# Performance work log

Hardware: AMD Instinct MI355X
Metric: run time of the kernel (lower is better)

Reference implementation:

```python
import jax, jax.numpy as jnp
import numpy as np

N_NODES, N_EDGES, HID = 30000, 480000, 128
N_GRAPHS, N_CLASSES = 128, 6
BN_EPS, ADD_SCORE = 1e-5, 0.5


def setup_inputs():
    key = jax.random.key(0)
    ks = jax.random.split(key, 12)
    g = lambda i, shape: jax.random.normal(ks[i], shape, jnp.float32) * 0.05
    return dict(
        x=jax.random.normal(ks[0], (N_NODES, HID), jnp.float32),
        edge_index=jax.random.randint(ks[1], (2, N_EDGES), 0, N_NODES, jnp.int32),
        batch=jnp.sort(jax.random.randint(ks[2], (N_NODES,), 0, N_GRAPHS, jnp.int32)),
        Wl=g(3, (6, HID, HID)), bl=jnp.zeros((6, HID), jnp.float32),
        Wr=g(4, (6, HID, HID)),
        gamma=jnp.ones((6, HID), jnp.float32), beta=jnp.zeros((6, HID), jnp.float32),
        Wlin=g(5, (3, HID, 2 * HID)), blin=jnp.zeros((3, HID), jnp.float32),
        Wp=g(6, (3, 2 * HID)), bp=jnp.zeros((3,), jnp.float32),
        Wf1=g(7, (HID, HID)), bf1=jnp.zeros((HID,), jnp.float32),
        Wf2=g(8, (N_CLASSES, HID)), bf2=jnp.zeros((N_CLASSES,), jnp.float32),
    )


def _sage(x, src, dst, emf, Wl_i, bl_i, Wr_i, N):
    # PyG SAGEConv: lin_l(mean_{j->i} x_j) + lin_r(x_i); emf masks dead edges
    msg = x[src] * emf[:, None]                              # [E,H]
    s = jax.ops.segment_sum(msg, dst, num_segments=N)
    c = jax.ops.segment_sum(emf, dst, num_segments=N)
    mean = s / jnp.maximum(c, 1.0)[:, None]
    return mean @ Wl_i.T + bl_i + x @ Wr_i.T


def _bn(x, g, b, nvf):
    # training-mode BatchNorm over valid (non-merged-away) nodes only
    cnt = jnp.maximum(nvf.sum(), 1.0)
    mu = (x * nvf[:, None]).sum(0) / cnt
    var = (((x - mu) ** 2) * nvf[:, None]).sum(0) / cnt
    return g * (x - mu) * jax.lax.rsqrt(var + BN_EPS) + b


def _edge_pool(x, src, dst, emb, nvb, Wp_i, bp_i, N, E):
    h = x.shape[1]
    # raw edge score = Linear(cat(x[src], x[dst]))
    raw = (x @ Wp_i[:h])[src] + (x @ Wp_i[h:])[dst] + bp_i   # [E]
    neg = jnp.finfo(x.dtype).min
    mx = jax.ops.segment_max(jnp.where(emb, raw, neg), dst, num_segments=N)
    z = jnp.where(emb, jnp.exp(jnp.where(emb, raw - mx[dst], 0.0)), 0.0)
    den = jax.ops.segment_sum(z, dst, num_segments=N)
    score = z / jnp.maximum(den, 1e-16)[dst] + ADD_SCORE     # softmax per dst + 0.5

    # greedy edge matching in descending score order (sequential, int-only carry)
    order = jnp.argsort(-jnp.where(emb, jax.lax.stop_gradient(score), -jnp.inf))

    def step(carry, i):
        matched, cluster, chosen = carry
        s, t = src[i], dst[i]
        ok = emb[i] & (~matched[s]) & (~matched[t]) & (s != t)
        rep, oth = jnp.minimum(s, t), jnp.maximum(s, t)
        matched = matched.at[s].set(matched[s] | ok)
        matched = matched.at[t].set(matched[t] | ok)
        cluster = cluster.at[oth].set(jnp.where(ok, rep, cluster[oth]))
        chosen = chosen.at[rep].set(jnp.where(ok, i, chosen[rep]))
        return (matched, cluster, chosen), None

    init = (~nvb, jnp.arange(N, dtype=jnp.int32), jnp.full((N,), -1, jnp.int32))
    (matched, cluster, chosen), _ = jax.lax.scan(step, init, order)

    # merged node = (x_s + x_t) * score(chosen edge); singleton score = 1
    nscore = jnp.where(chosen >= 0, score[jnp.maximum(chosen, 0)], 1.0)
    new_x = jax.ops.segment_sum(x, cluster, num_segments=N) * nscore[:, None]
    nvb2 = nvb & (cluster == jnp.arange(N, dtype=jnp.int32))
    # remap edges to cluster representatives; coalesce duplicates (self-loops kept, as PyG)
    key = jnp.where(emb, cluster[src] * N + cluster[dst], -1)  # N*N < 2**31
    uk = jnp.unique(key, size=E, fill_value=-1)
    emb2 = uk >= 0
    ukc = jnp.maximum(uk, 0)
    return new_x, ukc // N, ukc % N, emb2, nvb2


def reference(x, edge_index, batch, Wl, bl, Wr, gamma, beta, Wlin, blin, Wp, bp, Wf1, bf1, Wf2, bf2):
    N, E = x.shape[0], edge_index.shape[1]
    src, dst = edge_index[0], edge_index[1]
    emb = jnp.ones((E,), bool)   # edge-valid mask (fixed-shape graph coarsening)
    nvb = jnp.ones((N,), bool)   # node-valid mask
    for blk in range(3):
        emf, nvf = emb.astype(x.dtype), nvb.astype(x.dtype)
        i = 2 * blk
        h = _bn(jax.nn.relu(_sage(x, src, dst, emf, Wl[i], bl[i], Wr[i], N)), gamma[i], beta[i], nvf)
        h2 = _bn(jax.nn.relu(_sage(h, src, dst, emf, Wl[i + 1], bl[i + 1], Wr[i + 1], N)), gamma[i + 1], beta[i + 1], nvf)
        x = jnp.concatenate([h2, h], axis=1) @ Wlin[blk].T + blin[blk]  # dropout = identity (eval)
        x, src, dst, emb, nvb = _edge_pool(x, src, dst, emb, nvb, Wp[blk], bp[blk], N, E)
    nvf = nvb.astype(x.dtype)
    sums = jax.ops.segment_sum(x * nvf[:, None], batch, num_segments=N_GRAPHS)
    cnt = jax.ops.segment_sum(nvf, batch, num_segments=N_GRAPHS)
    pooled = sums / jnp.maximum(cnt, 1.0)[:, None]           # global_mean_pool
    hfc = jax.nn.relu(pooled @ Wf1.T + bf1)
    return jax.nn.log_softmax(hfc @ Wf2.T + bf2, axis=1)
```

## Files before the change

kernel.cpp:

```cpp
#include <hip/hip_runtime.h>
#include <stdint.h>

#define NN 30000
#define NE 480000
#define HID 128
#define NG 128
#define NC 6
#define BN_EPS 1e-5f
#define WPB 938
#define SLOTS 4
#define GPAD 132

typedef unsigned int u32;
typedef unsigned long long u64;

__device__ __forceinline__ u64 ent_key(int4 ent) {
  return ((u64)(u32)ent.y << 32) | (u32)ent.x;
}

__global__ void k_init(const int* __restrict__ ei, int* srcA, int* dstA, int* nvb,
                       int* scal, int* b3, int* i2, float* gbuf,
                       double* __restrict__ bnsum) {
  int t = blockIdx.x * 256 + threadIdx.x;
  if (t < NE) { srcA[t] = ei[t]; dstA[t] = ei[NE + t]; }
  if (t < NN) nvb[t] = 1;
  if (t < 2 * NN) { b3[t] = 0; i2[t] = 0; }
  if (t < NG * HID + NG) gbuf[t] = 0.f;
  if (t < 2 * HID) bnsum[t] = 0.0;
  if (t == 0) { scal[0] = NE; scal[1] = 0; }
}

__global__ void k_csr_count(const int* __restrict__ pE, const int* __restrict__ src,
                            const int* __restrict__ dst, int* __restrict__ cnt,
                            int* __restrict__ icnt, const int* __restrict__ nvb,
                            int* __restrict__ pcnt) {
  int t = blockIdx.x * 256 + threadIdx.x;
  if (t < NN && nvb[t]) atomicAdd(pcnt, 1);
  if (t < *pE) {
    int s = src[t], d = dst[t];
    atomicAdd(&cnt[d], 1);
    if (s != d) { atomicAdd(&icnt[s], 1); atomicAdd(&icnt[d], 1); }
  }
}

__global__ __launch_bounds__(1024) void k_scan2(const int* __restrict__ in0, int* __restrict__ out0,
                                                const int* __restrict__ in1, int* __restrict__ out1) {
  const int* in = blockIdx.x ? in1 : in0;
  int* out = blockIdx.x ? out1 : out0;
  __shared__ int part[1024];
  int t = threadIdx.x;
  int chunk = (NN + 1023) / 1024;
  int b = t * chunk, e = b + chunk;
  if (b > NN) b = NN;
  if (e > NN) e = NN;
  int s = 0;
  for (int i = b; i < e; i++) s += in[i];
  part[t] = s;
  __syncthreads();
  for (int off = 1; off < 1024; off <<= 1) {
    int v = (t >= off) ? part[t - off] : 0;
    __syncthreads();
    part[t] += v;
    __syncthreads();
  }
  int excl = (t == 0) ? 0 : part[t - 1];
  for (int i = b; i < e; i++) { out[i] = excl; excl += in[i]; }
  if (t == 0) out[NN] = part[1023];
}

__global__ void k_csr_scatter(const int* __restrict__ pE, const int* __restrict__ src,
                              const int* __restrict__ dst, const int* __restrict__ coff,
                              int* __restrict__ cursor, int* __restrict__ eids,
                              int* __restrict__ gsrc) {
  int e = blockIdx.x * 256 + threadIdx.x;
  if (e >= *pE) return;
  int d = dst[e];
  int pos = coff[d] + atomicAdd(&cursor[d], 1);
  eids[pos] = e;
  gsrc[pos] = src[e];
}

__global__ __launch_bounds__(256) void k_sage_gather(
    const int* __restrict__ coff, const int* __restrict__ gsrc,
    const float* __restrict__ x, float* __restrict__ mean) {
  int grp = threadIdx.x >> 5;
  int lane = threadIdx.x & 31;
  int n = blockIdx.x * 8 + grp;
  if (n >= NN) return;
  int b = coff[n], e2 = coff[n + 1];
  float4 acc = make_float4(0.f, 0.f, 0.f, 0.f);
  int i = b;
  for (; i + 1 < e2; i += 2) {
    int s0 = gsrc[i], s1 = gsrc[i + 1];
    float4 v0 = *(const float4*)(x + (size_t)s0 * HID + lane * 4);
    float4 v1 = *(const float4*)(x + (size_t)s1 * HID + lane * 4);
    acc.x += v0.x; acc.y += v0.y; acc.z += v0.z; acc.w += v0.w;
    acc.x += v1.x; acc.y += v1.y; acc.z += v1.z; acc.w += v1.w;
  }
  if (i < e2) {
    int s0 = gsrc[i];
    float4 v0 = *(const float4*)(x + (size_t)s0 * HID + lane * 4);
    acc.x += v0.x; acc.y += v0.y; acc.z += v0.z; acc.w += v0.w;
  }
  float inv = 1.0f / fmaxf((float)(e2 - b), 1.0f);
  acc.x *= inv; acc.y *= inv; acc.z *= inv; acc.w *= inv;
  *(float4*)(mean + (size_t)n * HID + lane * 4) = acc;
}

__global__ __launch_bounds__(256) void gemm_dual2(
    const float* __restrict__ A1, const float* __restrict__ W1,
    const float* __restrict__ A2, const float* __restrict__ W2,
    const float* __restrict__ bias, float* __restrict__ out,
    int M, int ldw, int relu, const int* __restrict__ nvb,
    double* __restrict__ bnsum, int dostats,
    const float* __restrict__ a1f, const float* __restrict__ c1f,
    const float* __restrict__ a2f, const float* __restrict__ c2f,
    const float* __restrict__ Wp, float* __restrict__ px1, float* __restrict__ px2) {
  __shared__ float Ast[16][GPAD];
  __shared__ float Ws[16][GPAD];
  int tid = threadIdx.x;
  int rg = tid >> 4, cg = tid & 15;
  int r0 = rg * 8, c0 = cg * 8;
  int row0 = blockIdx.x * 128;
  float acc[8][8];
#pragma unroll
  for (int a = 0; a < 8; a++)
#pragma unroll
    for (int bq = 0; bq < 8; bq++) acc[a][bq] = 0.f;

  for (int srcI = 0; srcI < 2; srcI++) {
    const float* A = srcI ? A2 : A1;
    const float* W = srcI ? W2 : W1;
    const float* fa = srcI ? a2f : a1f;
    const float* fc = srcI ? c2f : c1f;
    for (int kc = 0; kc < 128; kc += 16) {
#pragma unroll
      for (int i = 0; i < 2; i++) {
        int k = tid + i * 256;
        int r = k >> 2, c4 = (k & 3) << 2;
        int gr = row0 + r;
        float4 v = make_float4(0.f, 0.f, 0.f, 0.f);
        if (gr < M) v = *(const float4*)(A + (size_t)gr * 128 + kc + c4);
        if (fa) {
          float4 av = *(const float4*)(fa + kc + c4);
          float4 cv = *(const float4*)(fc + kc + c4);
          v.x = v.x * av.x + cv.x; v.y = v.y * av.y + cv.y;
          v.z = v.z * av.z + cv.z; v.w = v.w * av.w + cv.w;
        }
        Ast[c4 + 0][r] = v.x; Ast[c4 + 1][r] = v.y;
        Ast[c4 + 2][r] = v.z; Ast[c4 + 3][r] = v.w;
        float4 w = *(const float4*)(W + (size_t)r * ldw + kc + c4);
        Ws[c4 + 0][r] = w.x; Ws[c4 + 1][r] = w.y;
        Ws[c4 + 2][r] = w.z; Ws[c4 + 3][r] = w.w;
      }
      __syncthreads();
#pragma unroll
      for (int kk = 0; kk < 16; kk++) {
        float4 a0 = *(const float4*)(&Ast[kk][r0]);
        float4 a1 = *(const float4*)(&Ast[kk][r0 + 4]);
        float4 b0 = *(const float4*)(&Ws[kk][c0]);
        float4 b1 = *(const float4*)(&Ws[kk][c0 + 4]);
        float av[8] = {a0.x, a0.y, a0.z, a0.w, a1.x, a1.y, a1.z, a1.w};
        float bv[8] = {b0.x, b0.y, b0.z, b0.w, b1.x, b1.y, b1.z, b1.w};
#pragma unroll
        for (int rr = 0; rr < 8; rr++)
#pragma unroll
          for (int cc = 0; cc < 8; cc++) acc[rr][cc] += av[rr] * bv[cc];
      }
      __syncthreads();
    }
  }

  float wp1[8], wp2[8];
  if (Wp) {
#pragma unroll
    for (int cc = 0; cc < 8; cc++) { wp1[cc] = Wp[c0 + cc]; wp2[cc] = Wp[HID + c0 + cc]; }
  }
  float* part1 = (float*)Ast;
  float* part2 = (float*)Ws;
  float sCol[8], qCol[8];
#pragma unroll
  for (int cc = 0; cc < 8; cc++) { sCol[cc] = 0.f; qCol[cc] = 0.f; }
#pragma unroll
  for (int rr = 0; rr < 8; rr++) {
    int gr = row0 + r0 + rr;
    float p1 = 0.f, p2 = 0.f;
    if (gr < M) {
      int valid = dostats ? nvb[gr] : 0;
      float vv[8];
#pragma unroll
      for (int cc = 0; cc < 8; cc++) {
        float v = acc[rr][cc] + bias[c0 + cc];
        if (relu) v = fmaxf(v, 0.f);
        vv[cc] = v;
        if (valid) { sCol[cc] += v; qCol[cc] += v * v; }
        if (Wp) { p1 += v * wp1[cc]; p2 += v * wp2[cc]; }
      }
      *(float4*)(out + (size_t)gr * 128 + c0) = make_float4(vv[0], vv[1], vv[2], vv[3]);
      *(float4*)(out + (size_t)gr * 128 + c0 + 4) = make_float4(vv[4], vv[5], vv[6], vv[7]);
    }
    if (Wp) { part1[(r0 + rr) * 16 + cg] = p1; part2[(r0 + rr) * 16 + cg] = p2; }
  }
  if (Wp) {
    __syncthreads();
    if (tid < HID && row0 + tid < M) {
      float s1 = 0.f, s2 = 0.f;
#pragma unroll
      for (int g = 0; g < 16; g++) { s1 += part1[tid * 16 + g]; s2 += part2[tid * 16 + g]; }
      px1[row0 + tid] = s1;
      px2[row0 + tid] = s2;
    }
  }
  if (dostats) {
#pragma unroll
    for (int cc = 0; cc < 8; cc++) { Ast[rg][c0 + cc] = sCol[cc]; Ws[rg][c0 + cc] = qCol[cc]; }
    __syncthreads();
    if (tid < HID) {
      float s = 0.f, q = 0.f;
#pragma unroll
      for (int g = 0; g < 16; g++) { s += Ast[g][tid]; q += Ws[g][tid]; }
      atomicAdd(&bnsum[tid], (double)s);
      atomicAdd(&bnsum[HID + tid], (double)q);
    }
  }
}

__global__ void k_bnfold(double* __restrict__ bnsum, const int* __restrict__ cnt,
                         const float* __restrict__ gamma, const float* __restrict__ beta,
                         float* __restrict__ affa, float* __restrict__ affc) {
  int k = threadIdx.x;
  double c = (double)((*cnt > 1) ? *cnt : 1);
  double mu = bnsum[k] / c;
  double var = bnsum[HID + k] / c - mu * mu;
  if (var < 0.0) var = 0.0;
  double inv = 1.0 / sqrt(var + (double)BN_EPS);
  double a = (double)gamma[k] * inv;
  affa[k] = (float)a;
  affc[k] = (float)((double)beta[k] - mu * a);
  bnsum[k] = 0.0;
  bnsum[HID + k] = 0.0;
}

__global__ void k_edge_softmax_seed(
    const int* __restrict__ coff, const int* __restrict__ eids,
    const int* __restrict__ gsrc, const float* __restrict__ px1,
    const float* __restrict__ px2, const float* __restrict__ bp,
    float* __restrict__ score, u64* __restrict__ ekey, u64* __restrict__ S) {
  int n = blockIdx.x * 256 + threadIdx.x;
  if (n >= NN) return;
  S[n] = 0ull;
  int b = coff[n], e2 = coff[n + 1];
  if (b == e2) return;
  float p2 = px2[n] + *bp;
  float mx = -3.4e38f;
  for (int i = b; i < e2; i++) {
    float r = px1[gsrc[i]] + p2;
    mx = fmaxf(mx, r);
  }
  double den = 0.0;
  for (int i = b; i < e2; i++) {
    int eid = eids[i];
    float z = expf(px1[gsrc[i]] + p2 - mx);
    score[eid] = z;
    den += (double)z;
  }
  if (den < 1e-16) den = 1e-16;
  double invd = 1.0 / den;
  for (int i = b; i < e2; i++) {
    int eid = eids[i];
    float sc = (float)((double)score[eid] * invd) + 0.5f;
    score[eid] = sc;
    ekey[eid] = ((u64)__float_as_uint(sc) << 32) | (u64)(0xFFFFFFFFu - (u32)eid);
  }
}

__global__ void k_inc_scatter(const int* __restrict__ pE, const int* __restrict__ src,
                              const int* __restrict__ dst, const u64* __restrict__ ekey,
                              const int* __restrict__ ioff, int* __restrict__ icur,
                              int4* __restrict__ ielist) {
  int e = blockIdx.x * 256 + threadIdx.x;
  if (e >= *pE) return;
  int s = src[e], d = dst[e];
  if (s == d) return;
  u64 k = ekey[e];
  int4 ent;
  ent.x = (int)(u32)(k & 0xFFFFFFFFull);
  ent.y = (int)(u32)(k >> 32);
  ent.w = 0;
  ent.z = d;
  ielist[ioff[s] + atomicAdd(&icur[s], 1)] = ent;
  ent.z = s;
  ielist[ioff[d] + atomicAdd(&icur[d], 1)] = ent;
}

__global__ __launch_bounds__(256) void k_suitor(
    const int* __restrict__ ioff, const int4* __restrict__ ielist,
    const int* __restrict__ src, const int* __restrict__ dst,
    u64* __restrict__ S) {
  int wid = threadIdx.x >> 6;
  int lane = threadIdx.x & 63;
  int n = blockIdx.x * 4 + wid;
  if (n >= NN) return;
  int cur = n;
  while (cur >= 0) {
    int b = ioff[cur], e2 = ioff[cur + 1];
    int deg = e2 - b;
    if (deg == 0) break;
    if (deg <= 64 * SLOTS) {
      u64 key[SLOTS]; int pv[SLOTS];
#pragma unroll
      for (int s = 0; s < SLOTS; s++) {
        key[s] = 0; pv[s] = 0;
        int i = b + s * 64 + lane;
        if (i < e2) {
          int4 ent = ielist[i];
          key[s] = ent_key(ent);
          pv[s] = ent.z;
        }
      }
      long long res;
      for (;;) {
        u64 localBest = 0;
#pragma unroll
        for (int s = 0; s < SLOTS; s++) {
          if (!key[s]) continue;
          u64 sv = __hip_atomic_load(&S[pv[s]], __ATOMIC_RELAXED, __HIP_MEMORY_SCOPE_AGENT);
          if (sv >= key[s]) key[s] = 0;
          else if (key[s] > localBest) localBest = key[s];
        }
        u64 bestKey = localBest;
#pragma unroll
        for (int o = 32; o > 0; o >>= 1) {
          u64 other = __shfl_xor(bestKey, o, 64);
          if (other > bestKey) bestKey = other;
        }
        if (bestKey == 0) { res = -1; break; }
        int ms = -1;
#pragma unroll
        for (int s = 0; s < SLOTS; s++)
          if (ms < 0 && key[s] == bestKey) ms = s;
        u64 ball = __ballot(ms >= 0);
        int owner = (int)(__ffsll((long long)ball) - 1);
        long long r0 = -3;
        if (lane == owner) {
          int bv = pv[ms];
          u64 old = atomicMax(&S[bv], bestKey);
          if (old >= bestKey) { key[ms] = 0; r0 = -2; }
          else if (old == 0) r0 = -1;
          else {
            int eo = (int)(0xFFFFFFFFu - (u32)(old & 0xFFFFFFFFull));
            int so = src[eo], do_ = dst[eo];
            r0 = (so == bv) ? do_ : so;
          }
        }
        res = __shfl(r0, owner, 64);
        if (res != -2) break;
      }
      if (res < 0) break;
      cur = (int)res;
    } else {
      u64 bestKey = 0;
      for (int i = b + lane; i < e2; i += 64) {
        int4 ent = ielist[i];
        u64 k = ent_key(ent);
        if (k <= bestKey) continue;
        u64 sv = __hip_atomic_load(&S[ent.z], __ATOMIC_RELAXED, __HIP_MEMORY_SCOPE_AGENT);
        if (k > sv) bestKey = k;
      }
#pragma unroll
      for (int o = 32; o > 0; o >>= 1) {
        u64 other = __shfl_xor(bestKey, o, 64);
        if (other > bestKey) bestKey = other;
      }
      long long r0 = -1;
      if (bestKey != 0 && lane == 0) {
        int e = (int)(0xFFFFFFFFu - (u32)(bestKey & 0xFFFFFFFFull));
        int es = src[e], ed = dst[e];
        int bv = (es == cur) ? ed : es;
        u64 old = atomicMax(&S[bv], bestKey);
        if (old >= bestKey) r0 = cur;
        else if (old != 0) {
          int eo = (int)(0xFFFFFFFFu - (u32)(old & 0xFFFFFFFFull));
          int so = src[eo], do_ = dst[eo];
          r0 = (so == bv) ? do_ : so;
        }
      }
      long long res = (bestKey != 0) ? __shfl(r0, 0, 64) : -1;
      cur = (int)res;
    }
  }
}

__global__ __launch_bounds__(256) void k_new_x(
    const u64* __restrict__ S, const int* __restrict__ src, const int* __restrict__ dst,
    const float* __restrict__ score, const float* __restrict__ x,
    float* __restrict__ out, int* __restrict__ cluster,
    int* __restrict__ nvb, int* __restrict__ b3zero) {
  int gt = blockIdx.x * 256 + threadIdx.x;
  if (gt < 2 * NN) b3zero[gt] = 0;
  int grp = threadIdx.x >> 5;
  int lane = threadIdx.x & 31;
  int n = blockIdx.x * 8 + grp;
  if (n >= NN) return;
  u64 k = S[n];
  int partner = -1;
  int rep = n;
  bool isOth = false;
  float sc = 1.f;
  if (k) {
    int e = (int)(0xFFFFFFFFu - (u32)(k & 0xFFFFFFFFull));
    int s = src[e], d = dst[e];
    int other = (s == n) ? d : s;
    if (S[other] == k) {
      if (n > other) { isOth = true; rep = other; }
      else { partner = other; sc = score[e]; }
    }
  }
  float4 v = make_float4(0.f, 0.f, 0.f, 0.f);
  if (!isOth) {
    v = *(const float4*)(x + (size_t)n * HID + lane * 4);
    if (partner >= 0) {
      float4 w = *(const float4*)(x + (size_t)partner * HID + lane * 4);
      v.x = (v.x + w.x) * sc; v.y = (v.y + w.y) * sc;
      v.z = (v.z + w.z) * sc; v.w = (v.w + w.w) * sc;
    }
  }
  *(float4*)(out + (size_t)n * HID + lane * 4) = v;
  if (lane == 0) {
    cluster[n] = rep;
    nvb[n] = (nvb[n] && !isOth) ? 1 : 0;
  }
}

__global__ void k_bucket_count(const int* __restrict__ pE, const int* __restrict__ src,
                               const int* __restrict__ cluster, int* __restrict__ bcount) {
  int e = blockIdx.x * 256 + threadIdx.x;
  if (e >= *pE) return;
  atomicAdd(&bcount[cluster[src[e]]], 1);
}

__global__ __launch_bounds__(1024) void k_scan(const int* __restrict__ in, int* __restrict__ out,
                                               int n, int* totalDst) {
  __shared__ int part[1024];
  int t = threadIdx.x;
  int chunk = (n + 1023) / 1024;
  int b = t * chunk, e = b + chunk;
  if (b > n) b = n;
  if (e > n) e = n;
  int s = 0;
  for (int i = b; i < e; i++) s += in[i];
  part[t] = s;
  __syncthreads();
  for (int off = 1; off < 1024; off <<= 1) {
    int v = (t >= off) ? part[t - off] : 0;
    __syncthreads();
    part[t] += v;
    __syncthreads();
  }
  int excl = (t == 0) ? 0 : part[t - 1];
  int total = part[1023];
  for (int i = b; i < e; i++) { out[i] = excl; excl += in[i]; }
  if (t == 0) {
    out[n] = total;
    if (totalDst) *totalDst = total;
  }
}

__global__ void k_bucket_scatter(const int* __restrict__ pE, const int* __restrict__ src,
                                 const int* __restrict__ dst, const int* __restrict__ cluster,
                                 const int* __restrict__ boffs, int* __restrict__ bcursor,
                                 int* __restrict__ bucket) {
  int e = blockIdx.x * 256 + threadIdx.x;
  if (e >= *pE) return;
  int cs = cluster[src[e]], cd = cluster[dst[e]];
  int pos = boffs[cs] + atomicAdd(&bcursor[cs], 1);
  bucket[pos] = cd;
}

__global__ __launch_bounds__(256) void k_dedup_bitmap(
    const int* __restrict__ boffs, int* __restrict__ bucket,
    int* __restrict__ ucount) {
  __shared__ u32 bm[4][960];
  int wid = threadIdx.x >> 6;
  int lane = threadIdx.x & 63;
  int n = blockIdx.x * 4 + wid;
  int b = boffs[n], e = boffs[n + 1];
  for (int w = lane; w < 960; w += 64) bm[wid][w] = 0;
  __syncthreads();
  for (int i = b + lane; i < e; i += 64)
    atomicOr(&bm[wid][bucket[i] >> 5], 1u << (bucket[i] & 31));
  __syncthreads();
  int w0 = lane * 15;
  int w1 = w0 + 15; if (w1 > WPB) w1 = WPB;
  int cnt = 0;
  for (int w = w0; w < w1; w++) cnt += __popc(bm[wid][w]);
  int inc = cnt;
  for (int o = 1; o < 64; o <<= 1) { int v = __shfl_up(inc, o); if (lane >= o) inc += v; }
  int excl = inc - cnt;
  int total = __shfl(inc, 63);
  int pos = b + excl;
  for (int w = w0; w < w1; w++) {
    u32 v = bm[wid][w];
    while (v) { int bit = __ffs(v) - 1; bucket[pos++] = (w << 5) | bit; v &= v - 1; }
  }
  if (lane == 0) ucount[n] = total;
}

__global__ void k_emit(const int* __restrict__ boffs, const int* __restrict__ bucket,
                       const int* __restrict__ bucount, const int* __restrict__ bnoffs,
                       int* __restrict__ srcO, int* __restrict__ dstO,
                       int* __restrict__ b3zero, int* __restrict__ i2zero,
                       int* __restrict__ pcnt) {
  int t = blockIdx.x * 256 + threadIdx.x;
  int stride = gridDim.x * 256;
  for (int z = t; z < 2 * NN; z += stride) { b3zero[z] = 0; i2zero[z] = 0; }
  if (t == 0) *pcnt = 0;
  if (t >= NN) return;
  int u = bucount[t], b = boffs[t], o = bnoffs[t];
  for (int i = 0; i < u; i++) { srcO[o + i] = t; dstO[o + i] = bucket[b + i]; }
}

__global__ void k_graph_pool(const int* __restrict__ nvb, const int* __restrict__ batch,
                             const float* __restrict__ x, float* __restrict__ gsum,
                             float* __restrict__ gcnt) {
  int t = blockIdx.x * 256 + threadIdx.x;
  int n = t >> 2;
  if (n >= NN) return;
  if (!nvb[n]) return;
  int sub = t & 3;
  int g = batch[n];
  const float* xr = x + (size_t)n * HID + sub * 32;
  float* o = gsum + (size_t)g * HID + sub * 32;
#pragma unroll
  for (int i = 0; i < 8; i++) {
    float4 v = *(const float4*)(xr + i * 4);
    atomicAdd(o + i * 4 + 0, v.x); atomicAdd(o + i * 4 + 1, v.y);
    atomicAdd(o + i * 4 + 2, v.z); atomicAdd(o + i * 4 + 3, v.w);
  }
  if (sub == 0) atomicAdd(&gcnt[g], 1.0f);
}

__global__ __launch_bounds__(128) void k_head1(const float* __restrict__ gsum,
                                               const float* __restrict__ gcnt,
                                               const float* __restrict__ Wf1,
                                               const float* __restrict__ bf1,
                                               float* __restrict__ hfc) {
  int g = blockIdx.x;
  int j = threadIdx.x;
  __shared__ float p[HID];
  float c = fmaxf(gcnt[g], 1.f);
  p[j] = gsum[g * HID + j] / c;
  __syncthreads();
  float s = bf1[j];
  const float* w = Wf1 + (size_t)j * HID;
  for (int k = 0; k < HID; k++) s += p[k] * w[k];
  hfc[g * HID + j] = fmaxf(s, 0.f);
}

__global__ void k_head2(const float* __restrict__ hfc, const float* __restrict__ Wf2,
                        const float* __restrict__ bf2, float* __restrict__ out) {
  int g = blockIdx.x;
  int t = threadIdx.x;
  __shared__ float lg[NC];
  if (t < NC) {
    float s = bf2[t];
    const float* w = Wf2 + (size_t)t * HID;
    const float* h = hfc + (size_t)g * HID;
    for (int k = 0; k < HID; k++) s += h[k] * w[k];
    lg[t] = s;
  }
  __syncthreads();
  if (t == 0) {
    float m = lg[0];
    for (int c = 1; c < NC; c++) m = fmaxf(m, lg[c]);
    float se = 0.f;
    for (int c = 0; c < NC; c++) se += expf(lg[c] - m);
    float lse = m + logf(se);
    for (int c = 0; c < NC; c++) out[g * NC + c] = lg[c] - lse;
  }
}

extern "C" void kernel_launch(void* const* d_in, const int* in_sizes, int n_in,
                              void* d_out, int out_size, void* d_ws, size_t ws_size,
                              hipStream_t stream) {
  const float* x0 = (const float*)d_in[0];
  const int* ei = (const int*)d_in[1];
  const int* batch = (const int*)d_in[2];
  const float* Wl = (const float*)d_in[3];
  const float* bl = (const float*)d_in[4];
  const float* Wr = (const float*)d_in[5];
  const float* gamma = (const float*)d_in[6];
  const float* beta = (const float*)d_in[7];
  const float* Wlin = (const float*)d_in[8];
  const float* blin = (const float*)d_in[9];
  const float* Wp = (const float*)d_in[10];
  const float* bp = (const float*)d_in[11];
  const float* Wf1 = (const float*)d_in[12];
  const float* bf1 = (const float*)d_in[13];
  const float* Wf2 = (const float*)d_in[14];
  const float* bf2 = (const float*)d_in[15];
  float* out = (float*)d_out;

  const int NH = NN * HID;
  size_t off = 0;
  char* base = (char*)d_ws;
  auto carve = [&](size_t bytes) -> char* {
    char* p = base + off;
    off += (bytes + 255) & ~(size_t)255;
    return p;
  };
  float* xa = (float*)carve((size_t)NH * 4);
  float* xb = (float*)carve((size_t)NH * 4);
  float* xc = (float*)carve((size_t)NH * 4);
  float* xd = (float*)carve((size_t)NH * 4);
  int* srcA = (int*)carve((size_t)NE * 4);
  int* dstA = (int*)carve((size_t)NE * 4);
  int* srcB = (int*)carve((size_t)NE * 4);
  int* dstB = (int*)carve((size_t)NE * 4);
  float* escore = (float*)carve((size_t)NE * 4);
  int* ebucket = (int*)carve((size_t)NE * 4);
  int* eids = (int*)carve((size_t)NE * 4);
  int* gsrc = (int*)carve((size_t)NE * 4);
  u64* ekey = (u64*)carve((size_t)NE * 8);
  u64* S = (u64*)carve((size_t)NN * 8);
  float* npx1 = (float*)carve((size_t)NN * 4);
  float* npx2 = (float*)carve((size_t)NN * 4);
  int* ncluster = (int*)carve((size_t)NN * 4);
  int* nvb = (int*)carve((size_t)NN * 4);
  int* b3 = (int*)carve((size_t)3 * NN * 4);
  int* bcount = b3;
  int* bcursor = b3 + NN;
  int* bucount = b3 + 2 * NN;
  int* i2 = (int*)carve((size_t)2 * NN * 4);
  int* icnt = i2;
  int* icursor = i2 + NN;
  int* boffs = (int*)carve((size_t)(NN + 1) * 4);
  int* bnoffs = (int*)carve((size_t)(NN + 1) * 4);
  int* csroff = (int*)carve((size_t)(NN + 1) * 4);
  int* ioff = (int*)carve((size_t)(NN + 1) * 4);
  double* bnsum = (double*)carve((size_t)2 * HID * 8);
  float* affa1 = (float*)carve((size_t)HID * 4);
  float* affc1 = (float*)carve((size_t)HID * 4);
  float* affa2 = (float*)carve((size_t)HID * 4);
  float* affc2 = (float*)carve((size_t)HID * 4);
  float* gbuf = (float*)carve((size_t)(NG * HID + NG) * 4);
  float* gsum = gbuf;
  float* gcnt = gbuf + NG * HID;
  float* ghfc = (float*)carve((size_t)NG * HID * 4);
  int* scal = (int*)carve(64 * 4);
  (void)ws_size; (void)n_in; (void)in_sizes; (void)out_size;

  int4* ielist = (int4*)xc;

  int* pE = scal;
  int* pcnt = scal + 1;

  k_init<<<1875, 256, 0, stream>>>(ei, srcA, dstA, nvb, scal, b3, i2, gbuf, bnsum);

  int* srcC = srcA; int* dstC = dstA; int* srcN = srcB; int* dstN = dstB;
  float* xcur = xa;
  float* xtmp = xd;

  auto sage = [&](const float* xin, float* xout, int L, const float* fa, const float* fc) {
    k_sage_gather<<<3750, 256, 0, stream>>>(csroff, gsrc, xin, xtmp);
    gemm_dual2<<<235, 256, 0, stream>>>(xtmp, Wl + (size_t)L * HID * HID, xin,
                                        Wr + (size_t)L * HID * HID, bl + (size_t)L * HID,
                                        xout, NN, HID, 1, nvb, bnsum, 1,
                                        fa, fc, fa, fc, nullptr, nullptr, nullptr);
  };

  for (int b = 0; b < 3; b++) {
    const float* xin = (b == 0) ? x0 : (const float*)xcur;

    k_csr_count<<<1875, 256, 0, stream>>>(pE, srcC, dstC, bcount, icnt, nvb, pcnt);
    k_scan2<<<2, 1024, 0, stream>>>(bcount, csroff, icnt, ioff);
    k_csr_scatter<<<1875, 256, 0, stream>>>(pE, srcC, dstC, csroff, bcursor, eids, gsrc);

    sage(xin, xb, 2 * b, nullptr, nullptr);
    k_bnfold<<<1, 128, 0, stream>>>(bnsum, pcnt, gamma + (size_t)(2 * b) * HID,
                                    beta + (size_t)(2 * b) * HID, affa1, affc1);
    sage(xb, xc, 2 * b + 1, affa1, affc1);
    k_bnfold<<<1, 128, 0, stream>>>(bnsum, pcnt, gamma + (size_t)(2 * b + 1) * HID,
                                    beta + (size_t)(2 * b + 1) * HID, affa2, affc2);
    gemm_dual2<<<235, 256, 0, stream>>>(xc, Wlin + (size_t)b * HID * 2 * HID, xb,
                                        Wlin + (size_t)b * HID * 2 * HID + HID,
                                        blin + (size_t)b * HID, xcur, NN, 2 * HID, 0,
                                        nvb, bnsum, 0, affa2, affc2, affa1, affc1,
                                        Wp + (size_t)b * 2 * HID, npx1, npx2);

    k_edge_softmax_seed<<<118, 256, 0, stream>>>(csroff, eids, gsrc, npx1, npx2, bp + b,
                                                 escore, ekey, S);
    k_inc_scatter<<<1875, 256, 0, stream>>>(pE, srcC, dstC, ekey, ioff, icursor, ielist);
    k_suitor<<<7500, 256, 0, stream>>>(ioff, ielist, srcC, dstC, S);
    k_new_x<<<3750, 256, 0, stream>>>(S, srcC, dstC, escore, xcur, xtmp,
                                      ncluster, nvb, b3);

    if (b < 2) {
      k_bucket_count<<<1875, 256, 0, stream>>>(pE, srcC, ncluster, bcount);
      k_scan<<<1, 1024, 0, stream>>>(bcount, boffs, NN, (int*)nullptr);
      k_bucket_scatter<<<1875, 256, 0, stream>>>(pE, srcC, dstC, ncluster, boffs, bcursor,
                                                 ebucket);
      k_dedup_bitmap<<<7500, 256, 0, stream>>>(boffs, ebucket, bucount);
      k_scan<<<1, 1024, 0, stream>>>(bucount, bnoffs, NN, pE);
      k_emit<<<235, 256, 0, stream>>>(boffs, ebucket, bucount, bnoffs, srcN, dstN,
                                      b3, i2, pcnt);
      { int* t = srcC; srcC = srcN; srcN = t; t = dstC; dstC = dstN; dstN = t; }
    }
    { float* t = xcur; xcur = xtmp; xtmp = t; }
  }

  k_graph_pool<<<469, 256, 0, stream>>>(nvb, batch, xcur, gsum, gcnt);
  k_head1<<<NG, 128, 0, stream>>>(gsum, gcnt, Wf1, bf1, ghfc);
  k_head2<<<NG, 32, 0, stream>>>(ghfc, Wf2, bf2, out);
}
```

Before: 2.504 ms.

## Fuse incidence scatter into softmax kernel and CSR counting into edge emit

Removes the separate k_inc_scatter pass and the ekey buffer by writing incidence-list entries directly from the per-node softmax loop. Degree counting for the next block's CSR moves into k_emit and runs once up front for block 0, so the per-block k_csr_count launch goes away. The valid-node counter is now maintained in k_new_x (reset in the softmax kernel), and zeroing of b3/i2 moves into the dedup kernel. This saves launches and edge-array passes, but the scatter now runs node-serially in 118 blocks and emit does per-edge atomics in a serial per-node loop, which may reduce parallelism.

```diff
diff --git a/kernel.cpp b/kernel.cpp
--- a/kernel.cpp
+++ b/kernel.cpp
@@ -27,20 +27,17 @@
   if (t < 2 * NN) { b3[t] = 0; i2[t] = 0; }
   if (t < NG * HID + NG) gbuf[t] = 0.f;
   if (t < 2 * HID) bnsum[t] = 0.0;
-  if (t == 0) { scal[0] = NE; scal[1] = 0; }
+  if (t == 0) { scal[0] = NE; scal[1] = NN; }
 }
 
 __global__ void k_csr_count(const int* __restrict__ pE, const int* __restrict__ src,
                             const int* __restrict__ dst, int* __restrict__ cnt,
-                            int* __restrict__ icnt, const int* __restrict__ nvb,
-                            int* __restrict__ pcnt) {
-  int t = blockIdx.x * 256 + threadIdx.x;
-  if (t < NN && nvb[t]) atomicAdd(pcnt, 1);
-  if (t < *pE) {
-    int s = src[t], d = dst[t];
-    atomicAdd(&cnt[d], 1);
-    if (s != d) { atomicAdd(&icnt[s], 1); atomicAdd(&icnt[d], 1); }
-  }
+                            int* __restrict__ icnt) {
+  int e = blockIdx.x * 256 + threadIdx.x;
+  if (e >= *pE) return;
+  int s = src[e], d = dst[e];
+  atomicAdd(&cnt[d], 1);
+  if (s != d) { atomicAdd(&icnt[s], 1); atomicAdd(&icnt[d], 1); }
 }
 
 __global__ __launch_bounds__(1024) void k_scan2(const int* __restrict__ in0, int* __restrict__ out0,
@@ -245,8 +242,11 @@
     const int* __restrict__ coff, const int* __restrict__ eids,
     const int* __restrict__ gsrc, const float* __restrict__ px1,
     const float* __restrict__ px2, const float* __restrict__ bp,
-    float* __restrict__ score, u64* __restrict__ ekey, u64* __restrict__ S) {
+    float* __restrict__ score, u64* __restrict__ S,
+    const int* __restrict__ ioff, int* __restrict__ icur,
+    int4* __restrict__ ielist, int* __restrict__ pcnt) {
   int n = blockIdx.x * 256 + threadIdx.x;
+  if (blockIdx.x == 0 && threadIdx.x == 0) *pcnt = 0;
   if (n >= NN) return;
   S[n] = 0ull;
   int b = coff[n], e2 = coff[n + 1];
@@ -270,27 +270,18 @@
     int eid = eids[i];
     float sc = (float)((double)score[eid] * invd) + 0.5f;
     score[eid] = sc;
-    ekey[eid] = ((u64)__float_as_uint(sc) << 32) | (u64)(0xFFFFFFFFu - (u32)eid);
-  }
-}
-
-__global__ void k_inc_scatter(const int* __restrict__ pE, const int* __restrict__ src,
-                              const int* __restrict__ dst, const u64* __restrict__ ekey,
-                              const int* __restrict__ ioff, int* __restrict__ icur,
-                              int4* __restrict__ ielist) {
-  int e = blockIdx.x * 256 + threadIdx.x;
-  if (e >= *pE) return;
-  int s = src[e], d = dst[e];
-  if (s == d) return;
-  u64 k = ekey[e];
-  int4 ent;
-  ent.x = (int)(u32)(k & 0xFFFFFFFFull);
-  ent.y = (int)(u32)(k >> 32);
-  ent.w = 0;
-  ent.z = d;
-  ielist[ioff[s] + atomicAdd(&icur[s], 1)] = ent;
-  ent.z = s;
-  ielist[ioff[d] + atomicAdd(&icur[d], 1)] = ent;
+    int s = gsrc[i];
+    if (s == n) continue;
+    u64 k = ((u64)__float_as_uint(sc) << 32) | (u64)(0xFFFFFFFFu - (u32)eid);
+    int4 ent;
+    ent.x = (int)(u32)(k & 0xFFFFFFFFull);
+    ent.y = (int)(u32)(k >> 32);
+    ent.w = 0;
+    ent.z = s;
+    ielist[ioff[n] + atomicAdd(&icur[n], 1)] = ent;
+    ent.z = n;
+    ielist[ioff[s] + atomicAdd(&icur[s], 1)] = ent;
+  }
 }
 
 __global__ __launch_bounds__(256) void k_suitor(
@@ -395,7 +386,7 @@
     const u64* __restrict__ S, const int* __restrict__ src, const int* __restrict__ dst,
     const float* __restrict__ score, const float* __restrict__ x,
     float* __restrict__ out, int* __restrict__ cluster,
-    int* __restrict__ nvb, int* __restrict__ b3zero) {
+    int* __restrict__ nvb, int* __restrict__ b3zero, int* __restrict__ pcnt) {
   int gt = blockIdx.x * 256 + threadIdx.x;
   if (gt < 2 * NN) b3zero[gt] = 0;
   int grp = threadIdx.x >> 5;
@@ -428,7 +419,9 @@
   *(float4*)(out + (size_t)n * HID + lane * 4) = v;
   if (lane == 0) {
     cluster[n] = rep;
-    nvb[n] = (nvb[n] && !isOth) ? 1 : 0;
+    int nv = (nvb[n] && !isOth) ? 1 : 0;
+    nvb[n] = nv;
+    if (nv) atomicAdd(pcnt, 1);
   }
 }
 
@@ -479,7 +472,9 @@
 
 __global__ __launch_bounds__(256) void k_dedup_bitmap(
     const int* __restrict__ boffs, int* __restrict__ bucket,
-    int* __restrict__ ucount) {
+    int* __restrict__ ucount, int* __restrict__ b3zero, int* __restrict__ i2zero) {
+  int gt = blockIdx.x * 256 + threadIdx.x;
+  for (int z = gt; z < 2 * NN; z += gridDim.x * 256) { b3zero[z] = 0; i2zero[z] = 0; }
   __shared__ u32 bm[4][960];
   int wid = threadIdx.x >> 6;
   int lane = threadIdx.x & 63;
@@ -509,15 +504,17 @@
 __global__ void k_emit(const int* __restrict__ boffs, const int* __restrict__ bucket,
                        const int* __restrict__ bucount, const int* __restrict__ bnoffs,
                        int* __restrict__ srcO, int* __restrict__ dstO,
-                       int* __restrict__ b3zero, int* __restrict__ i2zero,
-                       int* __restrict__ pcnt) {
+                       int* __restrict__ cnt, int* __restrict__ icnt) {
   int t = blockIdx.x * 256 + threadIdx.x;
-  int stride = gridDim.x * 256;
-  for (int z = t; z < 2 * NN; z += stride) { b3zero[z] = 0; i2zero[z] = 0; }
-  if (t == 0) *pcnt = 0;
   if (t >= NN) return;
   int u = bucount[t], b = boffs[t], o = bnoffs[t];
-  for (int i = 0; i < u; i++) { srcO[o + i] = t; dstO[o + i] = bucket[b + i]; }
+  for (int i = 0; i < u; i++) {
+    int d = bucket[b + i];
+    srcO[o + i] = t;
+    dstO[o + i] = d;
+    atomicAdd(&cnt[d], 1);
+    if (t != d) { atomicAdd(&icnt[t], 1); atomicAdd(&icnt[d], 1); }
+  }
 }
 
 __global__ void k_graph_pool(const int* __restrict__ nvb, const int* __restrict__ batch,
@@ -621,7 +618,6 @@
   int* ebucket = (int*)carve((size_t)NE * 4);
   int* eids = (int*)carve((size_t)NE * 4);
   int* gsrc = (int*)carve((size_t)NE * 4);
-  u64* ekey = (u64*)carve((size_t)NE * 8);
   u64* S = (u64*)carve((size_t)NN * 8);
   float* npx1 = (float*)carve((size_t)NN * 4);
   float* npx2 = (float*)carve((size_t)NN * 4);
@@ -656,6 +652,7 @@
   int* pcnt = scal + 1;
 
   k_init<<<1875, 256, 0, stream>>>(ei, srcA, dstA, nvb, scal, b3, i2, gbuf, bnsum);
+  k_csr_count<<<1875, 256, 0, stream>>>(pE, srcA, dstA, bcount, icnt);
 
   int* srcC = srcA; int* dstC = dstA; int* srcN = srcB; int* dstN = dstB;
   float* xcur = xa;
@@ -672,7 +669,6 @@
   for (int b = 0; b < 3; b++) {
     const float* xin = (b == 0) ? x0 : (const float*)xcur;
 
-    k_csr_count<<<1875, 256, 0, stream>>>(pE, srcC, dstC, bcount, icnt, nvb, pcnt);
     k_scan2<<<2, 1024, 0, stream>>>(bcount, csroff, icnt, ioff);
     k_csr_scatter<<<1875, 256, 0, stream>>>(pE, srcC, dstC, csroff, bcursor, eids, gsrc);
 
@@ -689,21 +685,20 @@
                                         Wp + (size_t)b * 2 * HID, npx1, npx2);
 
     k_edge_softmax_seed<<<118, 256, 0, stream>>>(csroff, eids, gsrc, npx1, npx2, bp + b,
-                                                 escore, ekey, S);
-    k_inc_scatter<<<1875, 256, 0, stream>>>(pE, srcC, dstC, ekey, ioff, icursor, ielist);
+                                                 escore, S, ioff, icursor, ielist, pcnt);
     k_suitor<<<7500, 256, 0, stream>>>(ioff, ielist, srcC, dstC, S);
     k_new_x<<<3750, 256, 0, stream>>>(S, srcC, dstC, escore, xcur, xtmp,
-                                      ncluster, nvb, b3);
+                                      ncluster, nvb, b3, pcnt);
 
     if (b < 2) {
       k_bucket_count<<<1875, 256, 0, stream>>>(pE, srcC, ncluster, bcount);
       k_scan<<<1, 1024, 0, stream>>>(bcount, boffs, NN, (int*)nullptr);
       k_bucket_scatter<<<1875, 256, 0, stream>>>(pE, srcC, dstC, ncluster, boffs, bcursor,
                                                  ebucket);
-      k_dedup_bitmap<<<7500, 256, 0, stream>>>(boffs, ebucket, bucount);
+      k_dedup_bitmap<<<7500, 256, 0, stream>>>(boffs, ebucket, bucount, b3, i2);
       k_scan<<<1, 1024, 0, stream>>>(bucount, bnoffs, NN, pE);
-      k_emit<<<235, 256, 0, stream>>>(boffs, ebucket, bucount, bnoffs, srcN, dstN,
-                                      b3, i2, pcnt);
+      k_emit<<<118, 256, 0, stream>>>(boffs, ebucket, bucount, bnoffs, srcN, dstN,
+                                      bcount, icnt);
       { int* t = srcC; srcC = srcN; srcN = t; t = dstC; dstC = dstN; dstN = t; }
     }
     { float* t = xcur; xcur = xtmp; xtmp = t; }
```

Result: slower. 2.595 ms (+3.6%).
